# Kernel optimization log

Hardware: AMD Instinct MI355X
Metric: run time of the kernel (lower is better)

Reference implementation:

```python
import jax, jax.numpy as jnp
import numpy as np

N_NODES = 50000
IN_CH, HIDDEN, LATENT = 128, 256, 64
N_EDGES = 800000


def gcn_conv(x, edge_index, W, b, n_nodes):
    """PyG-style GCNConv: add self-loops, symmetric deg^{-1/2} normalization,
    linear transform, gather-scatter aggregation, bias."""
    loops = jnp.arange(n_nodes, dtype=edge_index.dtype)
    src = jnp.concatenate([edge_index[0], loops])  # [E+N]
    dst = jnp.concatenate([edge_index[1], loops])  # [E+N]
    deg = jax.ops.segment_sum(jnp.ones_like(dst, dtype=x.dtype), dst,
                              num_segments=n_nodes)  # [N]
    dinv = jnp.where(deg > 0, jax.lax.rsqrt(deg), 0.0)  # deg^{-1/2}
    h = x @ W  # [N, out] transform before propagation
    norm = dinv[src] * dinv[dst]  # [E+N]
    msg = h[src] * norm[:, None]  # gather + normalize, [E+N, out]
    out = jax.ops.segment_sum(msg, dst, num_segments=n_nodes)  # scatter-add
    return out + b


def setup_inputs() -> dict:
    key = jax.random.key(0)
    ks = jax.random.split(key, 10)
    x = jax.random.normal(ks[0], (N_NODES, IN_CH), dtype=jnp.float32)
    edge_index = jax.random.randint(ks[1], (2, N_EDGES), 0, N_NODES, dtype=jnp.int64)
    s = 0.05
    return {
        "x": x,
        "edge_index": edge_index,
        "W1": jax.random.normal(ks[2], (IN_CH, HIDDEN), dtype=jnp.float32) * s,
        "b1": jnp.zeros((HIDDEN,), dtype=jnp.float32),
        "W2": jax.random.normal(ks[3], (HIDDEN, LATENT), dtype=jnp.float32) * s,
        "b2": jnp.zeros((LATENT,), dtype=jnp.float32),
        "Wd1": jax.random.normal(ks[4], (LATENT, HIDDEN), dtype=jnp.float32) * s,
        "bd1": jnp.zeros((HIDDEN,), dtype=jnp.float32),
        "Wd2": jax.random.normal(ks[5], (HIDDEN, IN_CH), dtype=jnp.float32) * s,
        "bd2": jnp.zeros((IN_CH,), dtype=jnp.float32),
    }


def reference(x, edge_index, W1, b1, W2, b2, Wd1, bd1, Wd2, bd2):
    n = x.shape[0]
    # Encoder: two GCN layers
    h = jax.nn.relu(gcn_conv(x, edge_index, W1, b1, n))
    z = gcn_conv(h, edge_index, W2, b2, n)
    # Decoder: dense MLP
    d = jax.nn.relu(z @ Wd1 + bd1)
    return d @ Wd2 + bd2
```

## Files before the change

kernel.cpp:

```cpp
#include <hip/hip_runtime.h>


#define IN_CH  128
#define HIDDEN 256
#define LATENT 64

typedef unsigned short u16;
typedef unsigned int u32;
typedef float f32x4 __attribute__((ext_vector_type(4)));
typedef _Float16 f16x4 __attribute__((ext_vector_type(4)));
typedef _Float16 f16x8 __attribute__((ext_vector_type(8)));

static __device__ __forceinline__ float4 ld4(const float* p) {
    return *reinterpret_cast<const float4*>(p);
}
static __device__ __forceinline__ void acc4(float4& a, float4 v) {
    a.x += v.x; a.y += v.y; a.z += v.z; a.w += v.w;
}
static __device__ __forceinline__ f16x4 ldh4(const _Float16* p) {
    return *reinterpret_cast<const f16x4*>(p);
}
static __device__ __forceinline__ void acch(float4& a, f16x4 v) {
    a.x += (float)v[0]; a.y += (float)v[1]; a.z += (float)v[2]; a.w += (float)v[3];
}

static __device__ __forceinline__ long tix(int row, int k, int K) {
    return ((long)(row >> 4) * (K >> 3) + (k >> 3)) * 128 + ((row & 15) << 3) + (k & 7);
}

#define MFMA16(ACC, A, B)                                                      \
    ACC = __builtin_amdgcn_mfma_f32_16x16x32_f16(A, B, ACC, 0, 0, 0);


__global__ void hist_kernel(const int* __restrict__ ei, int E,
                            int* __restrict__ counts, int nper) {
    int part = blockIdx.x & 7;
    int e = (blockIdx.x >> 3) * 256 + threadIdx.x;
    if (e >= E) return;
    int d = ei[E + e];
    if ((unsigned)(d - part * nper) < (unsigned)nper) atomicAdd(&counts[d], 1);
}

__global__ void scan1_wsplit_kernel(
    const int* __restrict__ counts, int* __restrict__ rowptr,
    int* __restrict__ blocksums, float* __restrict__ dinv, int N, int nblk,
    const float* __restrict__ W1, const float* __restrict__ W2,
    const float* __restrict__ Wd1, const float* __restrict__ Wd2,
    _Float16* __restrict__ w1f, _Float16* __restrict__ w2f,
    _Float16* __restrict__ wd1f, _Float16* __restrict__ wd2f) {
    __shared__ int sh[256];
    int tid = threadIdx.x;
    if ((int)blockIdx.x < nblk) {
        int i = blockIdx.x * 256 + tid;
        int v = (i < N) ? counts[i] : 0;
        if (i < N) dinv[i] = rsqrtf((float)v + 1.0f);
        sh[tid] = v;
        __syncthreads();
        for (int off = 1; off < 256; off <<= 1) {
            int t = (tid >= off) ? sh[tid - off] : 0;
            __syncthreads();
            sh[tid] += t;
            __syncthreads();
        }
        if (i < N) rowptr[i] = sh[tid] - v;
        if (tid == 255) blocksums[blockIdx.x] = sh[255];
    } else {
        int idx = ((int)blockIdx.x - nblk) * 256 + tid;
        if (idx < 98304) {
            const float* W; _Float16* H; int K, Nn, base;
            if (idx < 32768)      { W = W1;  H = w1f;  K = 128; Nn = 256; base = idx; }
            else if (idx < 49152) { W = W2;  H = w2f;  K = 256; Nn = 64;  base = idx - 32768; }
            else if (idx < 65536) { W = Wd1; H = wd1f; K = 64;  Nn = 256; base = idx - 49152; }
            else                  { W = Wd2; H = wd2f; K = 256; Nn = 128; base = idx - 65536; }
            int k = base / Nn, n = base % Nn;
            H[tix(n, k, K)] = (_Float16)W[base];
        }
    }
}

__global__ void scan3_prescale_kernel(
    int* __restrict__ rowptr, const int* __restrict__ blocksums, int* __restrict__ next,
    const float* __restrict__ x, const float* __restrict__ dinv, _Float16* __restrict__ xsh,
    int N, int total4, int nblk) {
    __shared__ int sh[256];
    const int b = blockIdx.x;
    const int tid = threadIdx.x;
    int boff = 0;
    if (b < nblk) {
        int s = 0;
        for (int j = tid; j < b; j += 256) s += blocksums[j];
        sh[tid] = s;
        __syncthreads();
        for (int off = 128; off > 0; off >>= 1) {
            if (tid < off) sh[tid] += sh[tid + off];
            __syncthreads();
        }
        boff = sh[0];
        if (b == nblk - 1 && tid == 0) rowptr[N] = boff + blocksums[b];
    }
    int i = b * 256 + tid;
    if (b < nblk && i < N) {
        int r = rowptr[i] + boff;
        rowptr[i] = r;
        next[i] = r;
    }
    if (i < total4) {
        float s = dinv[i >> 5];
        float4 v = ld4(&x[(long)i * 4]);
        f16x4 h;
        h[0] = (_Float16)(v.x * s);
        h[1] = (_Float16)(v.y * s);
        h[2] = (_Float16)(v.z * s);
        h[3] = (_Float16)(v.w * s);
        *reinterpret_cast<f16x4*>(&xsh[(long)i * 4]) = h;
    }
}

__global__ void fill_kernel(const int* __restrict__ ei, int E,
                            int* __restrict__ next, int* __restrict__ col, int nper) {
    int part = blockIdx.x & 7;
    int e = (blockIdx.x >> 3) * 256 + threadIdx.x;
    if (e >= E) return;
    int d = ei[E + e];
    if ((unsigned)(d - part * nper) < (unsigned)nper) {
        int s = ei[e];
        int pos = atomicAdd(&next[d], 1);
        col[pos] = s;
    }
}


__global__ __launch_bounds__(256) void aggx_kernel(
    const _Float16* __restrict__ xsh, const int* __restrict__ rowptr,
    const int* __restrict__ col, const float* __restrict__ dinv,
    _Float16* __restrict__ xaf, int N) {
    int wid = threadIdx.x >> 6;
    int lane = threadIdx.x & 63;
    int node = blockIdx.x * 4 + wid;
    if (node >= N) return;
    int slot = lane >> 5;
    int c = (lane & 31) * 4;

    float4 a0 = make_float4(0.f, 0.f, 0.f, 0.f);
    float4 a1 = a0, a2 = a0, a3 = a0;
    if (slot == 0) acch(a0, ldh4(&xsh[(long)node * 128 + c]));

    int beg = rowptr[node];
    int end = rowptr[node + 1];
    for (int cb = beg; cb < end; cb += 64) {
        int cnt = min(64, end - cb);
        int cv = (lane < cnt) ? col[cb + lane] : 0;
        int full = cnt >> 1;
        int trips = (cnt + 1) >> 1;
        int t = 0;
        for (; t + 4 <= full; t += 4) {
            int j = slot + 2 * t;
            int s0 = __shfl(cv, j);
            int s1 = __shfl(cv, j + 2);
            int s2 = __shfl(cv, j + 4);
            int s3 = __shfl(cv, j + 6);
            f16x4 v0 = ldh4(&xsh[(long)s0 * 128 + c]);
            f16x4 v1 = ldh4(&xsh[(long)s1 * 128 + c]);
            f16x4 v2 = ldh4(&xsh[(long)s2 * 128 + c]);
            f16x4 v3 = ldh4(&xsh[(long)s3 * 128 + c]);
            acch(a0, v0); acch(a1, v1); acch(a2, v2); acch(a3, v3);
        }
        for (; t < trips; t++) {
            int j = slot + 2 * t;
            bool p = j < cnt;
            int s = __shfl(cv, p ? j : 0);
            if (p) acch(a0, ldh4(&xsh[(long)s * 128 + c]));
        }
    }
    acc4(a0, a1); acc4(a2, a3); acc4(a0, a2);
    a0.x += __shfl_xor(a0.x, 32);
    a0.y += __shfl_xor(a0.y, 32);
    a0.z += __shfl_xor(a0.z, 32);
    a0.w += __shfl_xor(a0.w, 32);
    if (slot == 0) {
        float di = dinv[node];
        f16x4 h;
        h[0] = (_Float16)(a0.x * di);
        h[1] = (_Float16)(a0.y * di);
        h[2] = (_Float16)(a0.z * di);
        h[3] = (_Float16)(a0.w * di);
        *(f16x4*)&xaf[tix(node, c, 128)] = h;
    }
}

__global__ __launch_bounds__(256) void agg64_kernel(
    const _Float16* __restrict__ zsh, const int* __restrict__ rowptr,
    const int* __restrict__ col, const float* __restrict__ dinv,
    const float* __restrict__ bias,
    _Float16* __restrict__ zf, int N) {
    int wid = threadIdx.x >> 6;
    int lane = threadIdx.x & 63;
    int node = blockIdx.x * 4 + wid;
    if (node >= N) return;
    int slot = lane >> 4;
    int c = (lane & 15) * 4;

    float4 a0 = make_float4(0.f, 0.f, 0.f, 0.f);
    float4 a1 = a0, a2 = a0, a3 = a0;
    if (slot == 0) acch(a0, ldh4(&zsh[(long)node * 64 + c]));

    int beg = rowptr[node];
    int end = rowptr[node + 1];
    for (int cb = beg; cb < end; cb += 64) {
        int cnt = min(64, end - cb);
        int cv = (lane < cnt) ? col[cb + lane] : 0;
        int full = cnt >> 2;
        int trips = (cnt + 3) >> 2;
        int t = 0;
        for (; t + 4 <= full; t += 4) {
            int j = slot + 4 * t;
            int s0 = __shfl(cv, j);
            int s1 = __shfl(cv, j + 4);
            int s2 = __shfl(cv, j + 8);
            int s3 = __shfl(cv, j + 12);
            f16x4 v0 = ldh4(&zsh[(long)s0 * 64 + c]);
            f16x4 v1 = ldh4(&zsh[(long)s1 * 64 + c]);
            f16x4 v2 = ldh4(&zsh[(long)s2 * 64 + c]);
            f16x4 v3 = ldh4(&zsh[(long)s3 * 64 + c]);
            acch(a0, v0); acch(a1, v1); acch(a2, v2); acch(a3, v3);
        }
        for (; t < trips; t++) {
            int j = slot + 4 * t;
            bool p = j < cnt;
            int s = __shfl(cv, p ? j : 0);
            if (p) acch(a0, ldh4(&zsh[(long)s * 64 + c]));
        }
    }
    acc4(a0, a1); acc4(a2, a3); acc4(a0, a2);
    a0.x += __shfl_xor(a0.x, 16); a0.x += __shfl_xor(a0.x, 32);
    a0.y += __shfl_xor(a0.y, 16); a0.y += __shfl_xor(a0.y, 32);
    a0.z += __shfl_xor(a0.z, 16); a0.z += __shfl_xor(a0.z, 32);
    a0.w += __shfl_xor(a0.w, 16); a0.w += __shfl_xor(a0.w, 32);
    if (slot == 0) {
        float di = dinv[node];
        float4 bi = ld4(&bias[c]);
        f16x4 h;
        h[0] = (_Float16)(a0.x * di + bi.x);
        h[1] = (_Float16)(a0.y * di + bi.y);
        h[2] = (_Float16)(a0.z * di + bi.z);
        h[3] = (_Float16)(a0.w * di + bi.w);
        *(f16x4*)&zf[tix(node, c, 64)] = h;
    }
}

__global__ __launch_bounds__(256) void enc_fused(
    const _Float16* __restrict__ xaf,
    const _Float16* __restrict__ w1f, const _Float16* __restrict__ w2f,
    const float* __restrict__ b1, const float* __restrict__ dinv,
    _Float16* __restrict__ zsh, int M) {
    __shared__ _Float16 o1f[32 * 256];

    const int tid = threadIdx.x;
    const int wid = tid >> 6, lane = tid & 63, quad = lane >> 4, lm = lane & 15;
    const int rt0 = blockIdx.x * 2;
    const int last_rt = (M >> 4) - 1;

    f32x4 acc[2][4];
#pragma unroll
    for (int i = 0; i < 2; i++)
#pragma unroll
        for (int j = 0; j < 4; j++) acc[i][j] = (f32x4){0.f, 0.f, 0.f, 0.f};

#pragma unroll
    for (int kc = 0; kc < 4; kc++) {
        const int kb = kc * 4 + quad;
        f16x8 a[2], b[4];
#pragma unroll
        for (int i = 0; i < 2; i++) {
            int rt = rt0 + i; rt = rt <= last_rt ? rt : last_rt;
            long o = ((long)rt * 16 + kb) * 128 + lm * 8;
            a[i] = *(const f16x8*)&xaf[o];
        }
#pragma unroll
        for (int j = 0; j < 4; j++) {
            long o = ((long)(wid * 4 + j) * 16 + kb) * 128 + lm * 8;
            b[j] = *(const f16x8*)&w1f[o];
        }
#pragma unroll
        for (int i = 0; i < 2; i++)
#pragma unroll
            for (int j = 0; j < 4; j++) { MFMA16(acc[i][j], a[i], b[j]); }
    }

#pragma unroll
    for (int i = 0; i < 2; i++)
#pragma unroll
        for (int j = 0; j < 4; j++) {
            int coln = wid * 64 + j * 16 + lm;
            float bi = b1[coln];
#pragma unroll
            for (int r = 0; r < 4; r++) {
                int row = i * 16 + quad * 4 + r;
                float v = fmaxf(acc[i][j][r] + bi, 0.f);
                int o = ((row >> 4) * 32 + (coln >> 3)) * 128 + ((row & 15) << 3) + (coln & 7);
                o1f[o] = (_Float16)v;
            }
        }
    __syncthreads();

    f32x4 acc2[2];
    acc2[0] = (f32x4){0.f, 0.f, 0.f, 0.f};
    acc2[1] = (f32x4){0.f, 0.f, 0.f, 0.f};
#pragma unroll
    for (int kc = 0; kc < 8; kc++) {
        const int kb = kc * 4 + quad;
        f16x8 a[2], b;
#pragma unroll
        for (int i = 0; i < 2; i++) {
            int o = (i * 32 + kb) * 128 + lm * 8;
            a[i] = *(const f16x8*)&o1f[o];
        }
        {
            long o = ((long)wid * 32 + kb) * 128 + lm * 8;
            b = *(const f16x8*)&w2f[o];
        }
#pragma unroll
        for (int i = 0; i < 2; i++) { MFMA16(acc2[i], a[i], b); }
    }
#pragma unroll
    for (int i = 0; i < 2; i++) {
        int coln = wid * 16 + lm;
#pragma unroll
        for (int r = 0; r < 4; r++) {
            int row = rt0 * 16 + i * 16 + quad * 4 + r;
            if (row < M) zsh[(long)row * 64 + coln] = (_Float16)(acc2[i][r] * dinv[row]);
        }
    }
}

__global__ __launch_bounds__(256) void dec_fused(
    const _Float16* __restrict__ zf,
    const _Float16* __restrict__ wd1f, const _Float16* __restrict__ wd2f,
    const float* __restrict__ bd1, const float* __restrict__ bd2,
    float* __restrict__ out, int M) {
    __shared__ _Float16 dsm[32 * 256];

    const int tid = threadIdx.x;
    const int wid = tid >> 6, lane = tid & 63, quad = lane >> 4, lm = lane & 15;
    const int rt0 = blockIdx.x * 2;
    const int last_rt = (M >> 4) - 1;

    f32x4 acc[2][4];
#pragma unroll
    for (int i = 0; i < 2; i++)
#pragma unroll
        for (int j = 0; j < 4; j++) acc[i][j] = (f32x4){0.f, 0.f, 0.f, 0.f};

#pragma unroll
    for (int kc = 0; kc < 2; kc++) {
        const int kb = kc * 4 + quad;
        f16x8 a[2], b[4];
#pragma unroll
        for (int i = 0; i < 2; i++) {
            int rt = rt0 + i; rt = rt <= last_rt ? rt : last_rt;
            long o = ((long)rt * 8 + kb) * 128 + lm * 8;
            a[i] = *(const f16x8*)&zf[o];
        }
#pragma unroll
        for (int j = 0; j < 4; j++) {
            long o = ((long)(wid * 4 + j) * 8 + kb) * 128 + lm * 8;
            b[j] = *(const f16x8*)&wd1f[o];
        }
#pragma unroll
        for (int i = 0; i < 2; i++)
#pragma unroll
            for (int j = 0; j < 4; j++) { MFMA16(acc[i][j], a[i], b[j]); }
    }

#pragma unroll
    for (int i = 0; i < 2; i++)
#pragma unroll
        for (int j = 0; j < 4; j++) {
            int coln = wid * 64 + j * 16 + lm;
            float bi = bd1[coln];
#pragma unroll
            for (int r = 0; r < 4; r++) {
                int row = i * 16 + quad * 4 + r;
                float v = fmaxf(acc[i][j][r] + bi, 0.f);
                int o = ((row >> 4) * 32 + (coln >> 3)) * 128 + ((row & 15) << 3) + (coln & 7);
                dsm[o] = (_Float16)v;
            }
        }
    __syncthreads();

    f32x4 acc2[2][2];
#pragma unroll
    for (int i = 0; i < 2; i++)
#pragma unroll
        for (int j = 0; j < 2; j++) acc2[i][j] = (f32x4){0.f, 0.f, 0.f, 0.f};
#pragma unroll
    for (int kc = 0; kc < 8; kc++) {
        const int kb = kc * 4 + quad;
        f16x8 a[2], b[2];
#pragma unroll
        for (int i = 0; i < 2; i++) {
            int o = (i * 32 + kb) * 128 + lm * 8;
            a[i] = *(const f16x8*)&dsm[o];
        }
#pragma unroll
        for (int j = 0; j < 2; j++) {
            long o = ((long)(wid * 2 + j) * 32 + kb) * 128 + lm * 8;
            b[j] = *(const f16x8*)&wd2f[o];
        }
#pragma unroll
        for (int i = 0; i < 2; i++)
#pragma unroll
            for (int j = 0; j < 2; j++) { MFMA16(acc2[i][j], a[i], b[j]); }
    }
#pragma unroll
    for (int i = 0; i < 2; i++)
#pragma unroll
        for (int j = 0; j < 2; j++) {
            int coln = wid * 32 + j * 16 + lm;
            float bi = bd2[coln];
#pragma unroll
            for (int r = 0; r < 4; r++) {
                int row = rt0 * 16 + i * 16 + quad * 4 + r;
                if (row < M) out[(long)row * 128 + coln] = acc2[i][j][r] + bi;
            }
        }
}


extern "C" void kernel_launch(void* const* d_in, const int* in_sizes, int n_in,
                              void* d_out, int out_size, void* d_ws, size_t ws_size,
                              hipStream_t stream) {
    const float* x        = (const float*)d_in[0];
    const int* ei         = (const int*)d_in[1];
    const float* W1       = (const float*)d_in[2];
    const float* b1       = (const float*)d_in[3];
    const float* W2       = (const float*)d_in[4];
    const float* b2       = (const float*)d_in[5];
    const float* Wd1      = (const float*)d_in[6];
    const float* bd1      = (const float*)d_in[7];
    const float* Wd2      = (const float*)d_in[8];
    const float* bd2      = (const float*)d_in[9];
    float* out            = (float*)d_out;

    const int N = in_sizes[0] / IN_CH;
    const int E = in_sizes[1] / 2;

    char* p = (char*)d_ws;
    auto alloc = [&](size_t bytes) {
        char* r = p;
        p += (bytes + 255) & ~(size_t)255;
        return r;
    };
    int*      counts    = (int*)     alloc((size_t)(N + 1) * 4);
    int*      rowptr    = (int*)     alloc((size_t)(N + 1) * 4);
    int*      nxt       = (int*)     alloc((size_t)N * 4);
    int*      blocksums = (int*)     alloc(256 * 4);
    float*    dinv      = (float*)   alloc((size_t)N * 4);
    int*      col       = (int*)     alloc((size_t)E * 4);
    _Float16* xsh       = (_Float16*)alloc((size_t)N * IN_CH * 2);
    _Float16* xaf       = (_Float16*)alloc((size_t)N * IN_CH * 2);
    _Float16* zsh       = (_Float16*)alloc((size_t)N * LATENT * 2);
    _Float16* zf        = (_Float16*)alloc((size_t)N * LATENT * 2);
    _Float16* w1f       = (_Float16*)alloc((size_t)IN_CH * HIDDEN * 2);
    _Float16* w2f       = (_Float16*)alloc((size_t)HIDDEN * LATENT * 2);
    _Float16* wd1f      = (_Float16*)alloc((size_t)LATENT * HIDDEN * 2);
    _Float16* wd2f      = (_Float16*)alloc((size_t)HIDDEN * IN_CH * 2);

    const int nblk = (N + 255) / 256;
    const int total4 = N * (IN_CH / 4);
    const int chunks = (E + 255) / 256;
    const int nper = (N + 7) / 8;
    const int fblk = (N + 31) / 32;

    hipMemsetAsync(counts, 0, (size_t)(N + 1) * 4, stream);
    hist_kernel<<<chunks * 8, 256, 0, stream>>>(ei, E, counts, nper);
    scan1_wsplit_kernel<<<nblk + 384, 256, 0, stream>>>(
        counts, rowptr, blocksums, dinv, N, nblk,
        W1, W2, Wd1, Wd2, w1f, w2f, wd1f, wd2f);
    scan3_prescale_kernel<<<(total4 + 255) / 256, 256, 0, stream>>>(
        rowptr, blocksums, nxt, x, dinv, xsh, N, total4, nblk);
    fill_kernel<<<chunks * 8, 256, 0, stream>>>(ei, E, nxt, col, nper);

    aggx_kernel<<<(N + 3) / 4, 256, 0, stream>>>(xsh, rowptr, col, dinv, xaf, N);
    enc_fused<<<fblk, 256, 0, stream>>>(xaf, w1f, w2f, b1, dinv, zsh, N);
    agg64_kernel<<<(N + 3) / 4, 256, 0, stream>>>(zsh, rowptr, col, dinv, b2, zf, N);
    dec_fused<<<fblk, 256, 0, stream>>>(zf, wd1f, wd2f, bd1, bd2, out, N);
}
```

Baseline: 260.6 us.

## Split gather feature tables into 32-channel slabs for L2-resident aggregation

Stores the prescaled input features and the latent features in a channel-sliced layout, with each 32-channel slab contiguous across all nodes. The aggregation kernels are rewritten so each block handles one slab for part of the nodes, with 8 edges gathered in parallel per wave at 64 bytes each. Block-index interleaving spreads the slabs across the XCDs so each slab's working set can stay in a smaller cache. Output stores become nontemporal. The trade-off is more cross-lane shuffle reductions, and neighbor indices are re-read once per slab.

```diff
diff --git a/kernel.cpp b/kernel.cpp
--- a/kernel.cpp
+++ b/kernel.cpp
@@ -7,6 +7,7 @@
 
 typedef unsigned short u16;
 typedef unsigned int u32;
+typedef unsigned long long u64;
 typedef float f32x4 __attribute__((ext_vector_type(4)));
 typedef _Float16 f16x4 __attribute__((ext_vector_type(4)));
 typedef _Float16 f16x8 __attribute__((ext_vector_type(8)));
@@ -22,6 +23,9 @@
 }
 static __device__ __forceinline__ void acch(float4& a, f16x4 v) {
     a.x += (float)v[0]; a.y += (float)v[1]; a.z += (float)v[2]; a.w += (float)v[3];
+}
+static __device__ __forceinline__ void sth4_nt(_Float16* p, f16x4 v) {
+    __builtin_nontemporal_store(__builtin_bit_cast(u64, v), (u64*)p);
 }
 
 static __device__ __forceinline__ long tix(int row, int k, int K) {
@@ -80,7 +84,7 @@
 
 __global__ void scan3_prescale_kernel(
     int* __restrict__ rowptr, const int* __restrict__ blocksums, int* __restrict__ next,
-    const float* __restrict__ x, const float* __restrict__ dinv, _Float16* __restrict__ xsh,
+    const float* __restrict__ x, const float* __restrict__ dinv, _Float16* __restrict__ xsq,
     int N, int total4, int nblk) {
     __shared__ int sh[256];
     const int b = blockIdx.x;
@@ -112,7 +116,10 @@
         h[1] = (_Float16)(v.y * s);
         h[2] = (_Float16)(v.z * s);
         h[3] = (_Float16)(v.w * s);
-        *reinterpret_cast<f16x4*>(&xsh[(long)i * 4]) = h;
+        int node = i >> 5;
+        int g = i & 31;
+        long o = ((long)(g >> 3) * N + node) * 32 + (g & 7) * 4;
+        *reinterpret_cast<f16x4*>(&xsq[o]) = h;
     }
 }
 
@@ -131,52 +138,66 @@
 
 
 __global__ __launch_bounds__(256) void aggx_kernel(
-    const _Float16* __restrict__ xsh, const int* __restrict__ rowptr,
+    const _Float16* __restrict__ xsq, const int* __restrict__ rowptr,
     const int* __restrict__ col, const float* __restrict__ dinv,
     _Float16* __restrict__ xaf, int N) {
-    int wid = threadIdx.x >> 6;
-    int lane = threadIdx.x & 63;
-    int node = blockIdx.x * 4 + wid;
+    const int part = blockIdx.x & 7;
+    const int q = part >> 1;
+    const int half = part & 1;
+    const int nh = (N + 1) >> 1;
+    const int li = (blockIdx.x >> 3) * 4 + (threadIdx.x >> 6);
+    if (li >= nh) return;
+    const int node = half * nh + li;
     if (node >= N) return;
-    int slot = lane >> 5;
-    int c = (lane & 31) * 4;
+    const int lane = threadIdx.x & 63;
+    const int slot = lane >> 3;
+    const int c = (lane & 7) * 4;
+    const _Float16* base = xsq + (long)q * N * 32;
 
     float4 a0 = make_float4(0.f, 0.f, 0.f, 0.f);
     float4 a1 = a0, a2 = a0, a3 = a0;
-    if (slot == 0) acch(a0, ldh4(&xsh[(long)node * 128 + c]));
+    if (slot == 0) acch(a0, ldh4(&base[(long)node * 32 + c]));
 
     int beg = rowptr[node];
     int end = rowptr[node + 1];
     for (int cb = beg; cb < end; cb += 64) {
         int cnt = min(64, end - cb);
         int cv = (lane < cnt) ? col[cb + lane] : 0;
-        int full = cnt >> 1;
-        int trips = (cnt + 1) >> 1;
+        int full = cnt >> 3;
+        int trips = (cnt + 7) >> 3;
         int t = 0;
         for (; t + 4 <= full; t += 4) {
-            int j = slot + 2 * t;
+            int j = slot + 8 * t;
             int s0 = __shfl(cv, j);
-            int s1 = __shfl(cv, j + 2);
-            int s2 = __shfl(cv, j + 4);
-            int s3 = __shfl(cv, j + 6);
-            f16x4 v0 = ldh4(&xsh[(long)s0 * 128 + c]);
-            f16x4 v1 = ldh4(&xsh[(long)s1 * 128 + c]);
-            f16x4 v2 = ldh4(&xsh[(long)s2 * 128 + c]);
-            f16x4 v3 = ldh4(&xsh[(long)s3 * 128 + c]);
+            int s1 = __shfl(cv, j + 8);
+            int s2 = __shfl(cv, j + 16);
+            int s3 = __shfl(cv, j + 24);
+            f16x4 v0 = ldh4(&base[(long)s0 * 32 + c]);
+            f16x4 v1 = ldh4(&base[(long)s1 * 32 + c]);
+            f16x4 v2 = ldh4(&base[(long)s2 * 32 + c]);
+            f16x4 v3 = ldh4(&base[(long)s3 * 32 + c]);
             acch(a0, v0); acch(a1, v1); acch(a2, v2); acch(a3, v3);
         }
+        for (; t + 2 <= full; t += 2) {
+            int j = slot + 8 * t;
+            int s0 = __shfl(cv, j);
+            int s1 = __shfl(cv, j + 8);
+            f16x4 v0 = ldh4(&base[(long)s0 * 32 + c]);
+            f16x4 v1 = ldh4(&base[(long)s1 * 32 + c]);
+            acch(a0, v0); acch(a1, v1);
+        }
         for (; t < trips; t++) {
-            int j = slot + 2 * t;
+            int j = slot + 8 * t;
             bool p = j < cnt;
             int s = __shfl(cv, p ? j : 0);
-            if (p) acch(a0, ldh4(&xsh[(long)s * 128 + c]));
+            if (p) acch(a0, ldh4(&base[(long)s * 32 + c]));
         }
     }
     acc4(a0, a1); acc4(a2, a3); acc4(a0, a2);
-    a0.x += __shfl_xor(a0.x, 32);
-    a0.y += __shfl_xor(a0.y, 32);
-    a0.z += __shfl_xor(a0.z, 32);
-    a0.w += __shfl_xor(a0.w, 32);
+    a0.x += __shfl_xor(a0.x, 8); a0.x += __shfl_xor(a0.x, 16); a0.x += __shfl_xor(a0.x, 32);
+    a0.y += __shfl_xor(a0.y, 8); a0.y += __shfl_xor(a0.y, 16); a0.y += __shfl_xor(a0.y, 32);
+    a0.z += __shfl_xor(a0.z, 8); a0.z += __shfl_xor(a0.z, 16); a0.z += __shfl_xor(a0.z, 32);
+    a0.w += __shfl_xor(a0.w, 8); a0.w += __shfl_xor(a0.w, 16); a0.w += __shfl_xor(a0.w, 32);
     if (slot == 0) {
         float di = dinv[node];
         f16x4 h;
@@ -184,67 +205,82 @@
         h[1] = (_Float16)(a0.y * di);
         h[2] = (_Float16)(a0.z * di);
         h[3] = (_Float16)(a0.w * di);
-        *(f16x4*)&xaf[tix(node, c, 128)] = h;
+        sth4_nt(&xaf[tix(node, q * 32 + c, 128)], h);
     }
 }
 
 __global__ __launch_bounds__(256) void agg64_kernel(
-    const _Float16* __restrict__ zsh, const int* __restrict__ rowptr,
+    const _Float16* __restrict__ zsq, const int* __restrict__ rowptr,
     const int* __restrict__ col, const float* __restrict__ dinv,
     const float* __restrict__ bias,
     _Float16* __restrict__ zf, int N) {
-    int wid = threadIdx.x >> 6;
-    int lane = threadIdx.x & 63;
-    int node = blockIdx.x * 4 + wid;
+    const int part = blockIdx.x & 7;
+    const int h8 = part >> 2;
+    const int qtr = part & 3;
+    const int nq = (N + 3) >> 2;
+    const int li = (blockIdx.x >> 3) * 4 + (threadIdx.x >> 6);
+    if (li >= nq) return;
+    const int node = qtr * nq + li;
     if (node >= N) return;
-    int slot = lane >> 4;
-    int c = (lane & 15) * 4;
+    const int lane = threadIdx.x & 63;
+    const int slot = lane >> 3;
+    const int c = (lane & 7) * 4;
+    const _Float16* base = zsq + (long)h8 * N * 32;
 
     float4 a0 = make_float4(0.f, 0.f, 0.f, 0.f);
     float4 a1 = a0, a2 = a0, a3 = a0;
-    if (slot == 0) acch(a0, ldh4(&zsh[(long)node * 64 + c]));
+    if (slot == 0) acch(a0, ldh4(&base[(long)node * 32 + c]));
 
     int beg = rowptr[node];
     int end = rowptr[node + 1];
     for (int cb = beg; cb < end; cb += 64) {
         int cnt = min(64, end - cb);
         int cv = (lane < cnt) ? col[cb + lane] : 0;
-        int full = cnt >> 2;
-        int trips = (cnt + 3) >> 2;
+        int full = cnt >> 3;
+        int trips = (cnt + 7) >> 3;
         int t = 0;
         for (; t + 4 <= full; t += 4) {
-            int j = slot + 4 * t;
+            int j = slot + 8 * t;
             int s0 = __shfl(cv, j);
-            int s1 = __shfl(cv, j + 4);
-            int s2 = __shfl(cv, j + 8);
-            int s3 = __shfl(cv, j + 12);
-            f16x4 v0 = ldh4(&zsh[(long)s0 * 64 + c]);
-            f16x4 v1 = ldh4(&zsh[(long)s1 * 64 + c]);
-            f16x4 v2 = ldh4(&zsh[(long)s2 * 64 + c]);
-            f16x4 v3 = ldh4(&zsh[(long)s3 * 64 + c]);
+            int s1 = __shfl(cv, j + 8);
+            int s2 = __shfl(cv, j + 16);
+            int s3 = __shfl(cv, j + 24);
+            f16x4 v0 = ldh4(&base[(long)s0 * 32 + c]);
+            f16x4 v1 = ldh4(&base[(long)s1 * 32 + c]);
+            f16x4 v2 = ldh4(&base[(long)s2 * 32 + c]);
+            f16x4 v3 = ldh4(&base[(long)s3 * 32 + c]);
             acch(a0, v0); acch(a1, v1); acch(a2, v2); acch(a3, v3);
         }
+        for (; t + 2 <= full; t += 2) {
+            int j = slot + 8 * t;
+            int s0 = __shfl(cv, j);
+            int s1 = __shfl(cv, j + 8);
+            f16x4 v0 = ldh4(&base[(long)s0 * 32 + c]);
+            f16x4 v1 = ldh4(&base[(long)s1 * 32 + c]);
+            acch(a0, v0); acch(a1, v1);
+        }
         for (; t < trips; t++) {
-            int j = slot + 4 * t;
+            int j = slot + 8 * t;
             bool p = j < cnt;
             int s = __shfl(cv, p ? j : 0);
-            if (p) acch(a0, ldh4(&zsh[(long)s * 64 + c]));
+            if (p) acch(a0, ldh4(&base[(long)s * 32 + c]));
         }
     }
     acc4(a0, a1); acc4(a2, a3); acc4(a0, a2);
-    a0.x += __shfl_xor(a0.x, 16); a0.x += __shfl_xor(a0.x, 32);
-    a0.y += __shfl_xor(a0.y, 16); a0.y += __shfl_xor(a0.y, 32);
-    a0.z += __shfl_xor(a0.z, 16); a0.z += __shfl_xor(a0.z, 32);
-    a0.w += __shfl_xor(a0.w, 16); a0.w += __shfl_xor(a0.w, 32);
+    a0.x += __shfl_xor(a0.x, 8); a0.x += __shfl_xor(a0.x, 16); a0.x += __shfl_xor(a0.x, 32);
+    a0.y += __shfl_xor(a0.y, 8); a0.y += __shfl_xor(a0.y, 16); a0.y += __shfl_xor(a0.y, 32);
+    a0.z += __shfl_xor(a0.z, 8); a0.z += __shfl_xor(a0.z, 16); a0.z += __shfl_xor(a0.z, 32);
+    a0.w += __shfl_xor(a0.w, 8); a0.w += __shfl_xor(a0.w, 16); a0.w += __shfl_xor(a0.w, 32);
     if (slot == 0) {
         float di = dinv[node];
-        float4 bi = ld4(&bias[c]);
+        int ch = h8 * 32 + c;
+        float4 bi = ld4(&bias[ch]);
         f16x4 h;
         h[0] = (_Float16)(a0.x * di + bi.x);
         h[1] = (_Float16)(a0.y * di + bi.y);
         h[2] = (_Float16)(a0.z * di + bi.z);
         h[3] = (_Float16)(a0.w * di + bi.w);
-        *(f16x4*)&zf[tix(node, c, 64)] = h;
+        sth4_nt(&zf[tix(node, ch, 64)], h);
     }
 }
 
@@ -252,7 +288,7 @@
     const _Float16* __restrict__ xaf,
     const _Float16* __restrict__ w1f, const _Float16* __restrict__ w2f,
     const float* __restrict__ b1, const float* __restrict__ dinv,
-    _Float16* __restrict__ zsh, int M) {
+    _Float16* __restrict__ zsq, int M) {
     __shared__ _Float16 o1f[32 * 256];
 
     const int tid = threadIdx.x;
@@ -328,7 +364,10 @@
 #pragma unroll
         for (int r = 0; r < 4; r++) {
             int row = rt0 * 16 + i * 16 + quad * 4 + r;
-            if (row < M) zsh[(long)row * 64 + coln] = (_Float16)(acc2[i][r] * dinv[row]);
+            if (row < M) {
+                long o = ((long)(coln >> 5) * M + row) * 32 + (coln & 31);
+                zsq[o] = (_Float16)(acc2[i][r] * dinv[row]);
+            }
         }
     }
 }
@@ -457,9 +496,9 @@
     int*      blocksums = (int*)     alloc(256 * 4);
     float*    dinv      = (float*)   alloc((size_t)N * 4);
     int*      col       = (int*)     alloc((size_t)E * 4);
-    _Float16* xsh       = (_Float16*)alloc((size_t)N * IN_CH * 2);
+    _Float16* xsq       = (_Float16*)alloc((size_t)N * IN_CH * 2);
     _Float16* xaf       = (_Float16*)alloc((size_t)N * IN_CH * 2);
-    _Float16* zsh       = (_Float16*)alloc((size_t)N * LATENT * 2);
+    _Float16* zsq       = (_Float16*)alloc((size_t)N * LATENT * 2);
     _Float16* zf        = (_Float16*)alloc((size_t)N * LATENT * 2);
     _Float16* w1f       = (_Float16*)alloc((size_t)IN_CH * HIDDEN * 2);
     _Float16* w2f       = (_Float16*)alloc((size_t)HIDDEN * LATENT * 2);
@@ -471,6 +510,8 @@
     const int chunks = (E + 255) / 256;
     const int nper = (N + 7) / 8;
     const int fblk = (N + 31) / 32;
+    const int nh = (N + 1) >> 1;
+    const int nq = (N + 3) >> 2;
 
     hipMemsetAsync(counts, 0, (size_t)(N + 1) * 4, stream);
     hist_kernel<<<chunks * 8, 256, 0, stream>>>(ei, E, counts, nper);
@@ -478,11 +519,11 @@
         counts, rowptr, blocksums, dinv, N, nblk,
         W1, W2, Wd1, Wd2, w1f, w2f, wd1f, wd2f);
     scan3_prescale_kernel<<<(total4 + 255) / 256, 256, 0, stream>>>(
-        rowptr, blocksums, nxt, x, dinv, xsh, N, total4, nblk);
+        rowptr, blocksums, nxt, x, dinv, xsq, N, total4, nblk);
     fill_kernel<<<chunks * 8, 256, 0, stream>>>(ei, E, nxt, col, nper);
 
-    aggx_kernel<<<(N + 3) / 4, 256, 0, stream>>>(xsh, rowptr, col, dinv, xaf, N);
-    enc_fused<<<fblk, 256, 0, stream>>>(xaf, w1f, w2f, b1, dinv, zsh, N);
-    agg64_kernel<<<(N + 3) / 4, 256, 0, stream>>>(zsh, rowptr, col, dinv, b2, zf, N);
+    aggx_kernel<<<((nh + 3) / 4) * 8, 256, 0, stream>>>(xsq, rowptr, col, dinv, xaf, N);
+    enc_fused<<<fblk, 256, 0, stream>>>(xaf, w1f, w2f, b1, dinv, zsq, N);
+    agg64_kernel<<<((nq + 3) / 4) * 8, 256, 0, stream>>>(zsq, rowptr, col, dinv, b2, zf, N);
     dec_fused<<<fblk, 256, 0, stream>>>(zf, wd1f, wd2f, bd1, bd2, out, N);
 }
```

New measurement: 306.5 us. 1.18x slower.
